# Performance work log

Measured on AMD Instinct MI355X. Metric: run time of the kernel, lower is better.

The kernel has to match this reference:

```python
import jax, jax.numpy as jnp
import numpy as np

B, T, D, U = 64, 512, 64, 256


def setup_inputs() -> dict:
    key = jax.random.key(0)
    k1, k2, k3, k4 = jax.random.split(key, 4)
    s = 0.05
    return {
        "x": jax.random.normal(k1, (B, T, D), dtype=jnp.float32),
        "W": jax.random.normal(k2, (D, 4 * U), dtype=jnp.float32) * s,
        "U": jax.random.normal(k3, (U, 4 * U), dtype=jnp.float32) * s,
        "b": jnp.zeros((4 * U,), dtype=jnp.float32),
        "dense_w": jax.random.normal(k4, (U, 1), dtype=jnp.float32) * s,
        "dense_b": jnp.zeros((1,), dtype=jnp.float32),
    }


def reference(x, W, U, b, dense_w, dense_b):
    # Keras LSTM with activation='relu', recurrent_activation='sigmoid'.
    # Gate packing order: i, f, c(g), o.
    units = U.shape[0]
    # Precompute input projections for all timesteps: [T, B, 4U]
    xz = jnp.einsum("btd,dg->tbg", x, W) + b

    def step(carry, xz_t):
        h, c = carry
        z = xz_t + h @ U  # [B, 4U]
        i = jax.nn.sigmoid(z[:, :units])
        f = jax.nn.sigmoid(z[:, units:2 * units])
        g = jax.nn.relu(z[:, 2 * units:3 * units])
        o = jax.nn.sigmoid(z[:, 3 * units:])
        c_new = f * c + i * g
        h_new = o * jax.nn.relu(c_new)
        return (h_new, c_new), h_new

    bsz = x.shape[0]
    h0 = jnp.zeros((bsz, units), dtype=x.dtype)
    c0 = jnp.zeros((bsz, units), dtype=x.dtype)
    _, hs = jax.lax.scan(step, (h0, c0), xz)  # hs: [T, B, U]
    hs = jnp.transpose(hs, (1, 0, 2))  # [B, T, U]
    sigma = jnp.squeeze(hs @ dense_w + dense_b, axis=-1)  # [B, T]
    return sigma
```

## Files before the change

### kernel.cpp

```cpp
#include <hip/hip_runtime.h>

#define B_  64
#define T_  512
#define D_  64
#define U_  256
#define G4  1024
#define NT  512

typedef _Float16 f16x8 __attribute__((ext_vector_type(8)));
typedef float    f32x4 __attribute__((ext_vector_type(4)));

__device__ __forceinline__ float sigmoidf_(float z) {
    return 1.f / (1.f + __expf(-z));
}

__global__ __launch_bounds__(256) void xz_kernel(const float* __restrict__ x,
                                                 const float* __restrict__ W,
                                                 const float* __restrict__ bias,
                                                 float* __restrict__ xz) {
    __shared__ float xt[16][D_];
    const int g    = blockIdx.x * 256 + threadIdx.x;
    const int row0 = blockIdx.y * 16;

    #pragma unroll
    for (int j = 0; j < 4; ++j) {
        int e = threadIdx.x + 256 * j;
        int r = e >> 6, d = e & 63;
        int row = row0 + r;
        int t = row >> 6, bb = row & 63;
        xt[r][d] = x[((size_t)bb * T_ + t) * D_ + d];
    }
    __syncthreads();

    float acc[16];
    #pragma unroll
    for (int r = 0; r < 16; ++r) acc[r] = 0.f;

    for (int d = 0; d < D_; ++d) {
        float wv = W[(size_t)d * G4 + g];
        #pragma unroll
        for (int r = 0; r < 16; ++r) acc[r] += xt[r][d] * wv;
    }

    float bg = bias[g];
    #pragma unroll
    for (int r = 0; r < 16; ++r)
        xz[(size_t)(row0 + r) * G4 + g] = acc[r] + bg;
}


struct Smem {
    _Float16 h16[256];
    float    z[G4];
    float    pd[U_];
    f16x8    bl[8][17][64];
};

__device__ __forceinline__ f16x8 load_bfrag(const float* __restrict__ Um,
                                            int ntg, int kt, int gg, int li) {
    const float* p = Um + (size_t)(32 * kt + 8 * gg) * G4 + 16 * ntg + li;
    f16x8 v;
    #pragma unroll
    for (int e = 0; e < 8; ++e) v[e] = (_Float16)p[(size_t)e * G4];
    return v;
}

#define FOR_AG(X) \
    X(2,1) X(2,2) X(2,3) X(2,4) X(2,5) X(2,6) X(2,7) \
    X(3,0) X(3,1) X(3,2) X(3,3) X(3,4) X(3,5) X(3,6) X(3,7) \
    X(4,0) X(4,1) X(4,2) X(4,3) X(4,4) X(4,5) X(4,6) X(4,7) \
    X(5,0) X(5,1) X(5,2) X(5,3) X(5,4) X(5,5) X(5,6) X(5,7) \
    X(6,0) X(6,1) X(6,2) X(6,3) X(6,4) X(6,5) X(6,6) X(6,7) \
    X(7,0) X(7,1) X(7,2) X(7,3) X(7,4) X(7,5) X(7,6) X(7,7)

#define DB(K,N) f16x8 bF_##K##_##N;
#define IB(K,N) bF_##K##_##N = load_bfrag(Um, w8 + (N), (K), gg, li);

#define MMV(N, BV) acc##N = __builtin_amdgcn_mfma_f32_16x16x32_f16(av, (BV), acc##N, 0, 0, 0);
#define MMR(K, N)  acc##N = __builtin_amdgcn_mfma_f32_16x16x32_f16(av, bF_##K##_##N, acc##N, 0, 0, 0);

#define MKLDS(KT, FB) { \
    f16x8 av = *(const f16x8*)&sm.h16[32 * (KT) + 8 * gg]; \
    { f16x8 bv = sm.bl[w][(FB)+0][lane]; MMV(0, bv) } \
    { f16x8 bv = sm.bl[w][(FB)+1][lane]; MMV(1, bv) } \
    { f16x8 bv = sm.bl[w][(FB)+2][lane]; MMV(2, bv) } \
    { f16x8 bv = sm.bl[w][(FB)+3][lane]; MMV(3, bv) } \
    { f16x8 bv = sm.bl[w][(FB)+4][lane]; MMV(4, bv) } \
    { f16x8 bv = sm.bl[w][(FB)+5][lane]; MMV(5, bv) } \
    { f16x8 bv = sm.bl[w][(FB)+6][lane]; MMV(6, bv) } \
    { f16x8 bv = sm.bl[w][(FB)+7][lane]; MMV(7, bv) } }

#define MKREG(KT) { \
    f16x8 av = *(const f16x8*)&sm.h16[32 * (KT) + 8 * gg]; \
    MMR(KT,0) MMR(KT,1) MMR(KT,2) MMR(KT,3) \
    MMR(KT,4) MMR(KT,5) MMR(KT,6) MMR(KT,7) }

__global__
__attribute__((amdgpu_flat_work_group_size(NT, NT), amdgpu_waves_per_eu(2, 2)))
void lstm_kernel(
        const float* __restrict__ Um,
        const float* __restrict__ dw,
        const float* __restrict__ dbp,
        const float* __restrict__ xz,
        float* __restrict__ out) {
    __shared__ Smem sm;

    const int tau  = threadIdx.x;
    const int b    = blockIdx.x;
    const int w    = tau >> 6;
    const int lane = tau & 63;
    const int gg   = (tau >> 4) & 3;
    const int li   = tau & 15;
    const int w8   = 8 * w;

    FOR_AG(DB)
    FOR_AG(IB)
    __builtin_amdgcn_sched_barrier(0);

    #pragma unroll
    for (int f = 0; f < 17; ++f) {
        const int kt = f >> 3, nt = f & 7;
        sm.bl[w][f][lane] = load_bfrag(Um, w8 + nt, kt, gg, li);
    }

    if (tau < U_) sm.h16[tau] = (_Float16)0.f;

    const float dwr = (tau < U_) ? dw[tau] : 0.f;
    const float db0 = dbp[0];
    float c_state = 0.f;

    float xq0 = 0.f, xq1 = 0.f, xq2 = 0.f, xq3 = 0.f;
    if (tau < U_) {
        const float* xp = xz + (size_t)b * G4;
        xq0 = xp[tau]; xq1 = xp[U_ + tau]; xq2 = xp[2 * U_ + tau]; xq3 = xp[3 * U_ + tau];
    }
    __syncthreads();

    for (int t = 0; t < T_; ++t) {
        const int tn = (t + 1 < T_) ? t + 1 : t;
        float xn0 = 0.f, xn1 = 0.f, xn2 = 0.f, xn3 = 0.f;
        if (tau < U_) {
            const float* xp = xz + ((size_t)tn * B_ + b) * G4;
            xn0 = xp[tau];
            xn1 = xp[U_ + tau];
            xn2 = xp[2 * U_ + tau];
            xn3 = xp[3 * U_ + tau];
        }
        __builtin_amdgcn_sched_barrier(0);

        f32x4 acc0 = {0.f,0.f,0.f,0.f}, acc1 = {0.f,0.f,0.f,0.f};
        f32x4 acc2 = {0.f,0.f,0.f,0.f}, acc3 = {0.f,0.f,0.f,0.f};
        f32x4 acc4 = {0.f,0.f,0.f,0.f}, acc5 = {0.f,0.f,0.f,0.f};
        f32x4 acc6 = {0.f,0.f,0.f,0.f}, acc7 = {0.f,0.f,0.f,0.f};

        MKLDS(0, 0)
        MKLDS(1, 8)
        {
            f16x8 av = *(const f16x8*)&sm.h16[64 + 8 * gg];
            { f16x8 bv = sm.bl[w][16][lane]; MMV(0, bv) }
            MMR(2,1) MMR(2,2) MMR(2,3) MMR(2,4) MMR(2,5) MMR(2,6) MMR(2,7)
        }
        MKREG(3) MKREG(4) MKREG(5) MKREG(6) MKREG(7)

        if (lane < 16) {
            const int zb = 128 * w + lane;
            sm.z[zb]       = acc0.x;  sm.z[zb + 16]  = acc1.x;
            sm.z[zb + 32]  = acc2.x;  sm.z[zb + 48]  = acc3.x;
            sm.z[zb + 64]  = acc4.x;  sm.z[zb + 80]  = acc5.x;
            sm.z[zb + 96]  = acc6.x;  sm.z[zb + 112] = acc7.x;
        }
        __syncthreads();

        if (tau < U_) {
            float zi = sm.z[tau]            + xq0;
            float zf = sm.z[U_ + tau]       + xq1;
            float zg = sm.z[2 * U_ + tau]   + xq2;
            float zo = sm.z[3 * U_ + tau]   + xq3;
            float ig = sigmoidf_(zi);
            float fg = sigmoidf_(zf);
            float gv = fmaxf(zg, 0.f);
            float og = sigmoidf_(zo);
            c_state = fg * c_state + ig * gv;
            float h = og * fmaxf(c_state, 0.f);
            sm.h16[tau] = (_Float16)h;
            sm.pd[tau]  = h * dwr;
        }
        __syncthreads();

        if (tau < 64) {
            float s = sm.pd[tau] + sm.pd[tau + 64] + sm.pd[tau + 128] + sm.pd[tau + 192];
            #pragma unroll
            for (int off = 32; off > 0; off >>= 1)
                s += __shfl_down(s, off);
            if (tau == 0) out[(size_t)b * T_ + t] = s + db0;
        }

        xq0 = xn0; xq1 = xn1; xq2 = xn2; xq3 = xn3;
    }
}

__global__ __launch_bounds__(1024) void lstm_fallback(
        const float* __restrict__ x,  const float* __restrict__ W,
        const float* __restrict__ Um, const float* __restrict__ bias,
        const float* __restrict__ dw, const float* __restrict__ dbp,
        float* __restrict__ out) {
    __shared__ float h_s[U_];
    __shared__ float z_s2[G4];
    __shared__ float pd_s2[U_];
    const int g = threadIdx.x;
    const int b = blockIdx.x;
    const float bg  = bias[g];
    const float dwr = (g < U_) ? dw[g] : 0.f;
    const float db0 = dbp[0];
    float c = 0.f;
    if (g < U_) h_s[g] = 0.f;
    __syncthreads();
    const float* Ucol = Um + g;
    for (int t = 0; t < T_; ++t) {
        float acc = bg;
        const float* xrow = x + ((size_t)b * T_ + t) * D_;
        for (int d = 0; d < D_; ++d) acc += xrow[d] * W[(size_t)d * G4 + g];
        for (int k = 0; k < U_; ++k) acc += h_s[k] * Ucol[(size_t)k * G4];
        z_s2[g] = acc;
        __syncthreads();
        if (g < U_) {
            float ig = sigmoidf_(z_s2[g]);
            float fg = sigmoidf_(z_s2[U_ + g]);
            float gg2 = fmaxf(z_s2[2 * U_ + g], 0.f);
            float og = sigmoidf_(z_s2[3 * U_ + g]);
            c = fg * c + ig * gg2;
            float h = og * fmaxf(c, 0.f);
            h_s[g] = h; pd_s2[g] = h * dwr;
        }
        __syncthreads();
        if (g < 64) {
            float s = pd_s2[g] + pd_s2[g + 64] + pd_s2[g + 128] + pd_s2[g + 192];
            #pragma unroll
            for (int off = 32; off > 0; off >>= 1) s += __shfl_down(s, off);
            if (g == 0) out[(size_t)b * T_ + t] = s + db0;
        }
        __syncthreads();
    }
}

extern "C" void kernel_launch(void* const* d_in, const int* in_sizes, int n_in,
                              void* d_out, int out_size, void* d_ws, size_t ws_size,
                              hipStream_t stream) {
    const float* x    = (const float*)d_in[0];
    const float* W    = (const float*)d_in[1];
    const float* Um   = (const float*)d_in[2];
    const float* bias = (const float*)d_in[3];
    const float* dw   = (const float*)d_in[4];
    const float* db   = (const float*)d_in[5];
    float* out = (float*)d_out;

    const size_t need = (size_t)T_ * B_ * G4 * sizeof(float);
    if (ws_size >= need) {
        float* xz = (float*)d_ws;
        dim3 gridX(G4 / 256, (T_ * B_) / 16);
        xz_kernel<<<gridX, 256, 0, stream>>>(x, W, bias, xz);
        lstm_kernel<<<B_, NT, 0, stream>>>(Um, dw, db, xz, out);
    } else {
        lstm_fallback<<<B_, 1024, 0, stream>>>(x, W, Um, bias, dw, db, out);
    }
}
```

Before: 936.8 us.

## Stream pre-packed fp16 recurrent weights from global memory instead of registers

```diff
diff --git a/kernel.cpp b/kernel.cpp
--- a/kernel.cpp
+++ b/kernel.cpp
@@ -12,6 +12,15 @@
 
 __device__ __forceinline__ float sigmoidf_(float z) {
     return 1.f / (1.f + __expf(-z));
+}
+
+__device__ __forceinline__ f16x8 load_bfrag(const float* __restrict__ Um,
+                                            int ntg, int kt, int gg, int li) {
+    const float* p = Um + (size_t)(32 * kt + 8 * gg) * G4 + 16 * ntg + li;
+    f16x8 v;
+    #pragma unroll
+    for (int e = 0; e < 8; ++e) v[e] = (_Float16)p[(size_t)e * G4];
+    return v;
 }
 
 __global__ __launch_bounds__(256) void xz_kernel(const float* __restrict__ x,
@@ -48,6 +57,19 @@
         xz[(size_t)(row0 + r) * G4 + g] = acc[r] + bg;
 }
 
+__global__ __launch_bounds__(256) void pack_kernel(const float* __restrict__ Um,
+                                                   f16x8* __restrict__ pk) {
+    const int idx  = blockIdx.x * 256 + threadIdx.x;
+    const int lane = idx & 63;
+    const int fid  = idx >> 6;
+    const int nt   = fid & 7;
+    const int kt   = (fid >> 3) & 7;
+    const int w    = fid >> 6;
+    const int gg   = (lane >> 4) & 3;
+    const int li   = lane & 15;
+    pk[idx] = load_bfrag(Um, 8 * w + nt, kt, gg, li);
+}
+
 
 struct Smem {
     _Float16 h16[256];
@@ -56,28 +78,9 @@
     f16x8    bl[8][17][64];
 };
 
-__device__ __forceinline__ f16x8 load_bfrag(const float* __restrict__ Um,
-                                            int ntg, int kt, int gg, int li) {
-    const float* p = Um + (size_t)(32 * kt + 8 * gg) * G4 + 16 * ntg + li;
-    f16x8 v;
-    #pragma unroll
-    for (int e = 0; e < 8; ++e) v[e] = (_Float16)p[(size_t)e * G4];
-    return v;
-}
-
-#define FOR_AG(X) \
-    X(2,1) X(2,2) X(2,3) X(2,4) X(2,5) X(2,6) X(2,7) \
-    X(3,0) X(3,1) X(3,2) X(3,3) X(3,4) X(3,5) X(3,6) X(3,7) \
-    X(4,0) X(4,1) X(4,2) X(4,3) X(4,4) X(4,5) X(4,6) X(4,7) \
-    X(5,0) X(5,1) X(5,2) X(5,3) X(5,4) X(5,5) X(5,6) X(5,7) \
-    X(6,0) X(6,1) X(6,2) X(6,3) X(6,4) X(6,5) X(6,6) X(6,7) \
-    X(7,0) X(7,1) X(7,2) X(7,3) X(7,4) X(7,5) X(7,6) X(7,7)
-
-#define DB(K,N) f16x8 bF_##K##_##N;
-#define IB(K,N) bF_##K##_##N = load_bfrag(Um, w8 + (N), (K), gg, li);
-
 #define MMV(N, BV) acc##N = __builtin_amdgcn_mfma_f32_16x16x32_f16(av, (BV), acc##N, 0, 0, 0);
-#define MMR(K, N)  acc##N = __builtin_amdgcn_mfma_f32_16x16x32_f16(av, bF_##K##_##N, acc##N, 0, 0, 0);
+#define MMS(K, N)  { f16x8 bv = pkp[(((K) << 3) | (N)) << 6]; \
+                     acc##N = __builtin_amdgcn_mfma_f32_16x16x32_f16(av, bv, acc##N, 0, 0, 0); }
 
 #define MKLDS(KT, FB) { \
     f16x8 av = *(const f16x8*)&sm.h16[32 * (KT) + 8 * gg]; \
@@ -90,10 +93,10 @@
     { f16x8 bv = sm.bl[w][(FB)+6][lane]; MMV(6, bv) } \
     { f16x8 bv = sm.bl[w][(FB)+7][lane]; MMV(7, bv) } }
 
-#define MKREG(KT) { \
+#define MKSTRM(KT) { \
     f16x8 av = *(const f16x8*)&sm.h16[32 * (KT) + 8 * gg]; \
-    MMR(KT,0) MMR(KT,1) MMR(KT,2) MMR(KT,3) \
-    MMR(KT,4) MMR(KT,5) MMR(KT,6) MMR(KT,7) }
+    MMS(KT,0) MMS(KT,1) MMS(KT,2) MMS(KT,3) \
+    MMS(KT,4) MMS(KT,5) MMS(KT,6) MMS(KT,7) }
 
 __global__
 __attribute__((amdgpu_flat_work_group_size(NT, NT), amdgpu_waves_per_eu(2, 2)))
@@ -102,6 +105,7 @@
         const float* __restrict__ dw,
         const float* __restrict__ dbp,
         const float* __restrict__ xz,
+        const f16x8* __restrict__ pk,
         float* __restrict__ out) {
     __shared__ Smem sm;
 
@@ -113,9 +117,7 @@
     const int li   = tau & 15;
     const int w8   = 8 * w;
 
-    FOR_AG(DB)
-    FOR_AG(IB)
-    __builtin_amdgcn_sched_barrier(0);
+    const f16x8* __restrict__ pkp = pk + (((size_t)w << 6) << 6) + lane;
 
     #pragma unroll
     for (int f = 0; f < 17; ++f) {
@@ -145,6 +147,122 @@
             xn1 = xp[U_ + tau];
             xn2 = xp[2 * U_ + tau];
             xn3 = xp[3 * U_ + tau];
+        }
+
+        f32x4 acc0 = {0.f,0.f,0.f,0.f}, acc1 = {0.f,0.f,0.f,0.f};
+        f32x4 acc2 = {0.f,0.f,0.f,0.f}, acc3 = {0.f,0.f,0.f,0.f};
+        f32x4 acc4 = {0.f,0.f,0.f,0.f}, acc5 = {0.f,0.f,0.f,0.f};
+        f32x4 acc6 = {0.f,0.f,0.f,0.f}, acc7 = {0.f,0.f,0.f,0.f};
+
+        MKLDS(0, 0)
+        MKLDS(1, 8)
+        {
+            f16x8 av = *(const f16x8*)&sm.h16[64 + 8 * gg];
+            { f16x8 bv = sm.bl[w][16][lane]; MMV(0, bv) }
+            MMS(2,1) MMS(2,2) MMS(2,3) MMS(2,4) MMS(2,5) MMS(2,6) MMS(2,7)
+        }
+        MKSTRM(3) MKSTRM(4) MKSTRM(5) MKSTRM(6) MKSTRM(7)
+
+        if (lane < 16) {
+            const int zb = 128 * w + lane;
+            sm.z[zb]       = acc0.x;  sm.z[zb + 16]  = acc1.x;
+            sm.z[zb + 32]  = acc2.x;  sm.z[zb + 48]  = acc3.x;
+            sm.z[zb + 64]  = acc4.x;  sm.z[zb + 80]  = acc5.x;
+            sm.z[zb + 96]  = acc6.x;  sm.z[zb + 112] = acc7.x;
+        }
+        __syncthreads();
+
+        if (tau < U_) {
+            float zi = sm.z[tau]            + xq0;
+            float zf = sm.z[U_ + tau]       + xq1;
+            float zg = sm.z[2 * U_ + tau]   + xq2;
+            float zo = sm.z[3 * U_ + tau]   + xq3;
+            float ig = sigmoidf_(zi);
+            float fg = sigmoidf_(zf);
+            float gv = fmaxf(zg, 0.f);
+            float og = sigmoidf_(zo);
+            c_state = fg * c_state + ig * gv;
+            float h = og * fmaxf(c_state, 0.f);
+            sm.h16[tau] = (_Float16)h;
+            sm.pd[tau]  = h * dwr;
+        }
+        __syncthreads();
+
+        if (tau < 64) {
+            float s = sm.pd[tau] + sm.pd[tau + 64] + sm.pd[tau + 128] + sm.pd[tau + 192];
+            #pragma unroll
+            for (int off = 32; off > 0; off >>= 1)
+                s += __shfl_down(s, off);
+            if (tau == 0) out[(size_t)b * T_ + t] = s + db0;
+        }
+
+        xq0 = xn0; xq1 = xn1; xq2 = xn2; xq3 = xn3;
+    }
+}
+
+#define FOR_AG(X) \
+    X(2,1) X(2,2) X(2,3) X(2,4) X(2,5) X(2,6) X(2,7) \
+    X(3,0) X(3,1) X(3,2) X(3,3) X(3,4) X(3,5) X(3,6) X(3,7) \
+    X(4,0) X(4,1) X(4,2) X(4,3) X(4,4) X(4,5) X(4,6) X(4,7) \
+    X(5,0) X(5,1) X(5,2) X(5,3) X(5,4) X(5,5) X(5,6) X(5,7) \
+    X(6,0) X(6,1) X(6,2) X(6,3) X(6,4) X(6,5) X(6,6) X(6,7) \
+    X(7,0) X(7,1) X(7,2) X(7,3) X(7,4) X(7,5) X(7,6) X(7,7)
+
+#define DB(K,N) f16x8 bF_##K##_##N;
+#define IB(K,N) bF_##K##_##N = load_bfrag(Um, w8 + (N), (K), gg, li);
+#define MMR(K, N)  acc##N = __builtin_amdgcn_mfma_f32_16x16x32_f16(av, bF_##K##_##N, acc##N, 0, 0, 0);
+#define MKREG(KT) { \
+    f16x8 av = *(const f16x8*)&sm.h16[32 * (KT) + 8 * gg]; \
+    MMR(KT,0) MMR(KT,1) MMR(KT,2) MMR(KT,3) \
+    MMR(KT,4) MMR(KT,5) MMR(KT,6) MMR(KT,7) }
+
+__global__
+__attribute__((amdgpu_flat_work_group_size(NT, NT), amdgpu_waves_per_eu(2, 2)))
+void lstm_kernel_r15(
+        const float* __restrict__ Um,
+        const float* __restrict__ dw,
+        const float* __restrict__ dbp,
+        const float* __restrict__ xz,
+        float* __restrict__ out) {
+    __shared__ Smem sm;
+
+    const int tau  = threadIdx.x;
+    const int b    = blockIdx.x;
+    const int w    = tau >> 6;
+    const int lane = tau & 63;
+    const int gg   = (tau >> 4) & 3;
+    const int li   = tau & 15;
+    const int w8   = 8 * w;
+
+    FOR_AG(DB)
+    FOR_AG(IB)
+    __builtin_amdgcn_sched_barrier(0);
+
+    #pragma unroll
+    for (int f = 0; f < 17; ++f) {
+        const int kt = f >> 3, nt = f & 7;
+        sm.bl[w][f][lane] = load_bfrag(Um, w8 + nt, kt, gg, li);
+    }
+
+    if (tau < U_) sm.h16[tau] = (_Float16)0.f;
+
+    const float dwr = (tau < U_) ? dw[tau] : 0.f;
+    const float db0 = dbp[0];
+    float c_state = 0.f;
+
+    float xq0 = 0.f, xq1 = 0.f, xq2 = 0.f, xq3 = 0.f;
+    if (tau < U_) {
+        const float* xp = xz + (size_t)b * G4;
+        xq0 = xp[tau]; xq1 = xp[U_ + tau]; xq2 = xp[2 * U_ + tau]; xq3 = xp[3 * U_ + tau];
+    }
+    __syncthreads();
+
+    for (int t = 0; t < T_; ++t) {
+        const int tn = (t + 1 < T_) ? t + 1 : t;
+        float xn0 = 0.f, xn1 = 0.f, xn2 = 0.f, xn3 = 0.f;
+        if (tau < U_) {
+            const float* xp = xz + ((size_t)tn * B_ + b) * G4;
+            xn0 = xp[tau]; xn1 = xp[U_ + tau]; xn2 = xp[2 * U_ + tau]; xn3 = xp[3 * U_ + tau];
         }
         __builtin_amdgcn_sched_barrier(0);
 
@@ -254,12 +372,21 @@
     const float* db   = (const float*)d_in[5];
     float* out = (float*)d_out;
 
-    const size_t need = (size_t)T_ * B_ * G4 * sizeof(float);
-    if (ws_size >= need) {
+    const size_t need_xz = (size_t)T_ * B_ * G4 * sizeof(float);
+    const size_t pk_bytes = (size_t)512 * 64 * 16;
+
+    if (ws_size >= need_xz + pk_bytes) {
+        f16x8* pk = (f16x8*)d_ws;
+        float* xz = (float*)((char*)d_ws + pk_bytes);
+        dim3 gridX(G4 / 256, (T_ * B_) / 16);
+        xz_kernel<<<gridX, 256, 0, stream>>>(x, W, bias, xz);
+        pack_kernel<<<128, 256, 0, stream>>>(Um, pk);
+        lstm_kernel<<<B_, NT, 0, stream>>>(Um, dw, db, xz, pk, out);
+    } else if (ws_size >= need_xz) {
         float* xz = (float*)d_ws;
         dim3 gridX(G4 / 256, (T_ * B_) / 16);
         xz_kernel<<<gridX, 256, 0, stream>>>(x, W, bias, xz);
-        lstm_kernel<<<B_, NT, 0, stream>>>(Um, dw, db, xz, out);
+        lstm_kernel_r15<<<B_, NT, 0, stream>>>(Um, dw, db, xz, out);
     } else {
         lstm_fallback<<<B_, 1024, 0, stream>>>(x, W, Um, bias, dw, db, out);
     }
```

New measurement: 877.1 us. 6.4% less time.
